# Performance work log

Hardware: AMD Instinct MI355X
Metric: run time of the kernel (lower is better)

Reference implementation:

```python
import jax, jax.numpy as jnp
import numpy as np

N, E, D, H, C = 50000, 800000, 128, 2, 128
NEG_SLOPE = 0.2
EPS = 1e-16  # matches pyg softmax denominator epsilon


def _xavier(k, shape):
    fan_out, fan_in = shape[0], shape[-1]
    lim = float(np.sqrt(6.0 / (fan_in + fan_out)))
    return jax.random.uniform(k, shape, jnp.float32, -lim, lim)


def setup_inputs() -> dict:
    key = jax.random.key(0)
    ks = jax.random.split(key, 10)
    x = jax.random.normal(ks[0], (N, D), jnp.float32)
    edge_index = jax.random.randint(ks[1], (2, E), 0, N, dtype=jnp.int64)
    W1 = _xavier(ks[2], (H * C, D))
    att_l1 = _xavier(ks[3], (H, C))
    att_r1 = _xavier(ks[4], (H, C))
    W2 = _xavier(ks[5], (H * C, H * C))
    att_l2 = _xavier(ks[6], (H, C))
    att_r2 = _xavier(ks[7], (H, C))
    Wp1 = _xavier(ks[8], (C, H * C))
    bp1 = jnp.zeros((C,), jnp.float32)
    Wp2 = _xavier(ks[9], (C, C))
    bp2 = jnp.zeros((C,), jnp.float32)
    return dict(x=x, edge_index=edge_index, W1=W1, att_l1=att_l1, att_r1=att_r1,
                W2=W2, att_l2=att_l2, att_r2=att_r2, Wp1=Wp1, bp1=bp1, Wp2=Wp2, bp2=bp2)


def gat_layer(x, W, att_l, att_r, src, dst):
    n = x.shape[0]
    xl = (x @ W.T).reshape(n, H, C)              # lin_l == lin_r (shared)
    alpha_l = (xl * att_l).sum(-1)               # [n, H]
    alpha_r = (xl * att_r).sum(-1)               # [n, H]
    # per-edge attention logits: alpha_j (source) + alpha_i (dest)
    e = jax.nn.leaky_relu(alpha_l[src] + alpha_r[dst], NEG_SLOPE)  # [E, H]
    # segment softmax over incoming edges of each destination node
    m = jax.ops.segment_max(e, dst, num_segments=n)
    m = jnp.where(jnp.isfinite(m), m, 0.0)
    ex = jnp.exp(e - m[dst])
    denom = jax.ops.segment_sum(ex, dst, num_segments=n)
    a = ex / (denom[dst] + EPS)                  # [E, H]
    # weighted message + scatter-sum aggregation
    out = jax.ops.segment_sum(a[:, :, None] * xl[src], dst, num_segments=n)
    return out.reshape(n, H * C)


def reference(x, edge_index, W1, att_l1, att_r1, W2, att_l2, att_r2, Wp1, bp1, Wp2, bp2):
    src, dst = edge_index[0], edge_index[1]
    h = jax.nn.relu(gat_layer(x, W1, att_l1, att_r1, src, dst))   # dropout p=0 -> no-op
    h = jax.nn.relu(gat_layer(h, W2, att_l2, att_r2, src, dst))
    h = h @ Wp1.T + bp1
    h = h @ Wp2.T + bp2
    return h
```

## Files before the change

### kernel.cpp

```cpp
#include <hip/hip_runtime.h>
#include <hip/hip_bf16.h>
#include <stdint.h>

#define HC 256
#define NEG_SLOPE 0.2f
#define SOFTMAX_EPS 1e-16f
#define CSR_CAP 6144
#define PART_EPB 2048

typedef float floatx4 __attribute__((ext_vector_type(4)));
typedef _Float16 half8v __attribute__((ext_vector_type(8)));

__device__ __forceinline__ float in_load(const void* p, int i, int is_bf16) {
    return is_bf16 ? (float)((const __bf16*)p)[i] : ((const float*)p)[i];
}

__device__ __forceinline__ int edge_is64(const int* ei) {
    const uint32_t* ew = (const uint32_t*)ei;
    uint32_t myw = ew[2 * (threadIdx.x & 63) + 1];
    return (__ballot(myw != 0u) == 0ull) ? 1 : 0;
}
__device__ __forceinline__ int edge_src(const int* ei, int E, int e, int is64) {
    return is64 ? ei[2 * (size_t)e] : ei[e];
}
__device__ __forceinline__ int edge_dst(const int* ei, int E, int e, int is64) {
    return is64 ? ei[2 * (size_t)E + 2 * (size_t)e] : ei[(size_t)E + e];
}

__global__ void prep_partition_kernel(
    const void* __restrict__ xin, _Float16* __restrict__ x16, int nx,
    const void* __restrict__ w1,  _Float16* __restrict__ W1f, int n1,
    const void* __restrict__ w2,  _Float16* __restrict__ W2f, int n2,
    const void* __restrict__ wp1, _Float16* __restrict__ Wp1f, int n3,
    const void* __restrict__ wp2, _Float16* __restrict__ Wp2f, int n4,
    const void* __restrict__ a0, float* __restrict__ o0, int m0,
    const void* __restrict__ a1, float* __restrict__ o1, int m1,
    const void* __restrict__ a2, float* __restrict__ o2, int m2,
    const void* __restrict__ a3, float* __restrict__ o3, int m3,
    const void* __restrict__ a4, float* __restrict__ o4, int m4,
    const void* __restrict__ a5, float* __restrict__ o5, int m5,
    const int* __restrict__ ei, int E,
    int* __restrict__ bcnt, uint2* __restrict__ stage,
    int part_blocks) {
    if (blockIdx.x < part_blocks) {
        __shared__ int hist[256];
        __shared__ int chunk[256];
        const int t = threadIdx.x;
        const int is64 = edge_is64(ei);
        const int ebase = blockIdx.x * PART_EPB;
        hist[t] = 0;
        __syncthreads();
        for (int i = t; i < PART_EPB; i += 256) {
            const int e = ebase + i;
            if (e < E) atomicAdd(&hist[edge_dst(ei, E, e, is64) >> 8], 1);
        }
        __syncthreads();
        const int h = hist[t];
        if (h > 0) chunk[t] = atomicAdd(&bcnt[t * 16], h);
        __syncthreads();
        hist[t] = 0;
        __syncthreads();
        for (int i = t; i < PART_EPB; i += 256) {
            const int e = ebase + i;
            if (e < E) {
                const int s = edge_src(ei, E, e, is64);
                const int d = edge_dst(ei, E, e, is64);
                const int b = d >> 8;
                const int local = atomicAdd(&hist[b], 1);
                const int pos = chunk[b] + local;
                if (pos < CSR_CAP)
                    stage[(size_t)b * CSR_CAP + pos] =
                        make_uint2((uint32_t)s, (uint32_t)(d & 255));
            }
        }
        return;
    }
    const uint32_t w = ((const uint32_t*)xin)[threadIdx.x & 63];
    const uint32_t ef = ((w & 0xFFFFu) >> 7) & 0xFFu;
    const int fb = (__popcll(__ballot(ef >= 90u && ef <= 135u)) > 48) ? 1 : 0;

    int off = (blockIdx.x - part_blocks) * blockDim.x + threadIdx.x;
    if (off < nx) { x16[off] = (_Float16)in_load(xin, off, fb); return; }
    off -= nx;
    if (off < n1) { W1f[off] = (_Float16)in_load(w1, off, fb); return; }
    off -= n1;
    if (off < n2) { W2f[off] = (_Float16)in_load(w2, off, fb); return; }
    off -= n2;
    if (off < n3) { Wp1f[off] = (_Float16)in_load(wp1, off, fb); return; }
    off -= n3;
    if (off < n4) { Wp2f[off] = (_Float16)in_load(wp2, off, fb); return; }
    off -= n4;
    if (off < m0) { o0[off] = in_load(a0, off, fb); return; }
    off -= m0;
    if (off < m1) { o1[off] = in_load(a1, off, fb); return; }
    off -= m1;
    if (off < m2) { o2[off] = in_load(a2, off, fb); return; }
    off -= m2;
    if (off < m3) { o3[off] = in_load(a3, off, fb); return; }
    off -= m3;
    if (off < m4) { o4[off] = in_load(a4, off, fb); return; }
    off -= m4;
    if (off < m5) { o5[off] = in_load(a5, off, fb); return; }
}

__global__ __launch_bounds__(1024) void bucket_csr_kernel(
    const int* __restrict__ bcnt, const uint2* __restrict__ stage,
    int* __restrict__ row_ptr, int* __restrict__ esrc, int nb, int N) {
    __shared__ int scanv[256];
    __shared__ int hist[256];
    __shared__ int fill[256];
    __shared__ int wsum[4], wpre[4];
    const int b = blockIdx.x;
    const int t = threadIdx.x;
    const int lane = t & 63;
    const int wv = t >> 6;

    if (t < 256) {
        const int v = (t < nb) ? min(bcnt[t * 16], CSR_CAP) : 0;
        int inc = v;
#pragma unroll
        for (int off = 1; off < 64; off <<= 1) {
            int y = __shfl_up(inc, off);
            if (lane >= off) inc += y;
        }
        if (lane == 63) wsum[wv] = inc;
        __syncthreads();
        if (t == 0) {
            int run = 0;
#pragma unroll
            for (int ww = 0; ww < 4; ww++) { wpre[ww] = run; run += wsum[ww]; }
        }
        __syncthreads();
        const int excl = wpre[wv] + inc - v;
        scanv[t] = excl;
        if (b == 0 && t == nb - 1) row_ptr[N] = excl + v;
        hist[t] = 0;
    } else {
        __syncthreads();
        __syncthreads();
    }
    __syncthreads();

    const int base = scanv[b];
    const int cnt = min(bcnt[b * 16], CSR_CAP);
    const uint2* st = stage + (size_t)b * CSR_CAP;

    for (int i = t; i < cnt; i += 1024) atomicAdd(&hist[st[i].y], 1);
    __syncthreads();
    if (t < 256) {
        const int hv = hist[t];
        int hinc = hv;
#pragma unroll
        for (int off = 1; off < 64; off <<= 1) {
            int y = __shfl_up(hinc, off);
            if (lane >= off) hinc += y;
        }
        if (lane == 63) wsum[wv] = hinc;
        __syncthreads();
        if (t == 0) {
            int run = 0;
#pragma unroll
            for (int ww = 0; ww < 4; ww++) { wpre[ww] = run; run += wsum[ww]; }
        }
        __syncthreads();
        const int hexcl = wpre[wv] + hinc - hv;
        fill[t] = hexcl;
        const int node = (b << 8) + t;
        if (node < N) row_ptr[node] = base + hexcl;
    } else {
        __syncthreads();
        __syncthreads();
    }
    __syncthreads();
    for (int i = t; i < cnt; i += 1024) {
        const uint2 e = st[i];
        const int pos = atomicAdd(&fill[e.y], 1);
        esrc[base + pos] = (int)e.x;
    }
}

template <int KTEMP, int OTILES, bool BIAS, bool ALPHA, int OMODE>
__global__ __launch_bounds__(256, 2) void gemm_bt(
    const _Float16* __restrict__ A, const _Float16* __restrict__ B,
    const float* __restrict__ bias,
    float* __restrict__ C, _Float16* __restrict__ Cf16,
    const float* __restrict__ attl, const float* __restrict__ attr,
    float* __restrict__ al, float* __restrict__ ar,
    int M) {
    static_assert(!ALPHA || OTILES == 16, "alpha fusion assumes O=256");
    constexpr int TW = OTILES / 4;
    constexpr int O = OTILES * 16;
    const int tid = threadIdx.x;
    const int lane = tid & 63;
    const int wave = tid >> 6;
    const int mbase = blockIdx.x * 64;
    const int l15 = lane & 15;
    const int q = lane >> 4;
    const int kq = q * 8;
    const int wc = wave * TW * 16;

    int arow[4];
#pragma unroll
    for (int rt = 0; rt < 4; rt++) arow[rt] = min(mbase + rt * 16 + l15, M - 1);

    floatx4 acc[4][TW];
#pragma unroll
    for (int rt = 0; rt < 4; rt++)
#pragma unroll
        for (int tt = 0; tt < TW; tt++) acc[rt][tt] = (floatx4){0.f, 0.f, 0.f, 0.f};

    constexpr int KSTEPS = KTEMP / 32;
#pragma unroll
    for (int ks = 0; ks < KSTEPS; ks++) {
        const int k0 = ks * 32;
        half8v af[4], bf[TW];
#pragma unroll
        for (int rt = 0; rt < 4; rt++)
            af[rt] = *(const half8v*)(A + (size_t)arow[rt] * KTEMP + k0 + kq);
#pragma unroll
        for (int tt = 0; tt < TW; tt++)
            bf[tt] = *(const half8v*)(B + (size_t)(wc + tt * 16 + l15) * KTEMP + k0 + kq);
#pragma unroll
        for (int rt = 0; rt < 4; rt++)
#pragma unroll
            for (int tt = 0; tt < TW; tt++)
                acc[rt][tt] = __builtin_amdgcn_mfma_f32_16x16x32_f16(af[rt], bf[tt], acc[rt][tt], 0, 0, 0);
    }

    float aLp[4][4], aRp[4][4];
    if constexpr (ALPHA) {
#pragma unroll
        for (int rt = 0; rt < 4; rt++)
#pragma unroll
            for (int r = 0; r < 4; r++) { aLp[rt][r] = 0.f; aRp[rt][r] = 0.f; }
    }

#pragma unroll
    for (int rt = 0; rt < 4; rt++) {
        const int rb = mbase + rt * 16 + q * 4;
#pragma unroll
        for (int tt = 0; tt < TW; tt++) {
            const int gcol = wc + tt * 16 + l15;
            float atlv = 0.f, atrv = 0.f;
            if constexpr (ALPHA) { atlv = attl[gcol]; atrv = attr[gcol]; }
#pragma unroll
            for (int r = 0; r < 4; r++) {
                float v = acc[rt][tt][r];
                if constexpr (BIAS) v += bias[gcol];
                if constexpr (ALPHA) { aLp[rt][r] += v * atlv; aRp[rt][r] += v * atrv; }
                const int grow = rb + r;
                if (grow < M) {
                    if constexpr (OMODE == 2) {
                        Cf16[(size_t)grow * O + gcol] = (_Float16)v;
                    } else {
                        C[(size_t)grow * O + gcol] = v;
                    }
                }
            }
        }
    }

    if constexpr (ALPHA) {
        __shared__ float sAL[4][64], sAR[4][64];
#pragma unroll
        for (int rt = 0; rt < 4; rt++)
#pragma unroll
            for (int r = 0; r < 4; r++) {
                float vl = aLp[rt][r], vr = aRp[rt][r];
                vl += __shfl_xor(vl, 1); vl += __shfl_xor(vl, 2);
                vl += __shfl_xor(vl, 4); vl += __shfl_xor(vl, 8);
                vr += __shfl_xor(vr, 1); vr += __shfl_xor(vr, 2);
                vr += __shfl_xor(vr, 4); vr += __shfl_xor(vr, 8);
                if (l15 == 0) {
                    sAL[wave][rt * 16 + q * 4 + r] = vl;
                    sAR[wave][rt * 16 + q * 4 + r] = vr;
                }
            }
        __syncthreads();
        if (tid < 64) {
            const int grow = mbase + tid;
            if (grow < M) {
                al[2 * grow]     = sAL[0][tid] + sAL[1][tid];
                al[2 * grow + 1] = sAL[2][tid] + sAL[3][tid];
                ar[2 * grow]     = sAR[0][tid] + sAR[1][tid];
                ar[2 * grow + 1] = sAR[2][tid] + sAR[3][tid];
            }
        }
    }
}

__global__ __launch_bounds__(256, 2) void proj_fused_kernel(
    const _Float16* __restrict__ A, const _Float16* __restrict__ B1,
    const float* __restrict__ b1, const _Float16* __restrict__ B2,
    const float* __restrict__ b2, float* __restrict__ out, int M) {
    __shared__ _Float16 plds[64 * 128];
    const int tid = threadIdx.x;
    const int lane = tid & 63;
    const int wave = tid >> 6;
    const int mbase = blockIdx.x * 64;
    const int l15 = lane & 15;
    const int q = lane >> 4;
    const int kq = q * 8;
    const int wc = wave * 32;

    int arow[4];
#pragma unroll
    for (int rt = 0; rt < 4; rt++) arow[rt] = min(mbase + rt * 16 + l15, M - 1);

    floatx4 acc[4][2];
#pragma unroll
    for (int rt = 0; rt < 4; rt++)
#pragma unroll
        for (int tt = 0; tt < 2; tt++) acc[rt][tt] = (floatx4){0.f, 0.f, 0.f, 0.f};
#pragma unroll
    for (int ks = 0; ks < 8; ks++) {
        const int k0 = ks * 32;
        half8v af[4], bf[2];
#pragma unroll
        for (int rt = 0; rt < 4; rt++)
            af[rt] = *(const half8v*)(A + (size_t)arow[rt] * 256 + k0 + kq);
#pragma unroll
        for (int tt = 0; tt < 2; tt++)
            bf[tt] = *(const half8v*)(B1 + (size_t)(wc + tt * 16 + l15) * 256 + k0 + kq);
#pragma unroll
        for (int rt = 0; rt < 4; rt++)
#pragma unroll
            for (int tt = 0; tt < 2; tt++)
                acc[rt][tt] = __builtin_amdgcn_mfma_f32_16x16x32_f16(af[rt], bf[tt], acc[rt][tt], 0, 0, 0);
    }
#pragma unroll
    for (int rt = 0; rt < 4; rt++) {
#pragma unroll
        for (int tt = 0; tt < 2; tt++) {
            const int col = wc + tt * 16 + l15;
            const float bv = b1[col];
#pragma unroll
            for (int r = 0; r < 4; r++) {
                const int row = rt * 16 + q * 4 + r;
                const int byt = row * 256 + ((((col >> 3) ^ (row & 15)) << 4)) + (col & 7) * 2;
                *(_Float16*)((char*)plds + byt) = (_Float16)(acc[rt][tt][r] + bv);
            }
        }
    }
    __syncthreads();

    floatx4 acc2[4][2];
#pragma unroll
    for (int rt = 0; rt < 4; rt++)
#pragma unroll
        for (int tt = 0; tt < 2; tt++) acc2[rt][tt] = (floatx4){0.f, 0.f, 0.f, 0.f};
#pragma unroll
    for (int ks = 0; ks < 4; ks++) {
        half8v af[4], bf[2];
#pragma unroll
        for (int rt = 0; rt < 4; rt++) {
            const int row = rt * 16 + l15;
            const int byt = (row << 8) + (((ks * 4 + q) ^ l15) << 4);
            af[rt] = *(const half8v*)((const char*)plds + byt);
        }
#pragma unroll
        for (int tt = 0; tt < 2; tt++)
            bf[tt] = *(const half8v*)(B2 + (size_t)(wc + tt * 16 + l15) * 128 + ks * 32 + kq);
#pragma unroll
        for (int rt = 0; rt < 4; rt++)
#pragma unroll
            for (int tt = 0; tt < 2; tt++)
                acc2[rt][tt] = __builtin_amdgcn_mfma_f32_16x16x32_f16(af[rt], bf[tt], acc2[rt][tt], 0, 0, 0);
    }
#pragma unroll
    for (int rt = 0; rt < 4; rt++) {
        const int rb = mbase + rt * 16 + q * 4;
#pragma unroll
        for (int tt = 0; tt < 2; tt++) {
            const int gcol = wc + tt * 16 + l15;
            const float bv = b2[gcol];
#pragma unroll
            for (int r = 0; r < 4; r++) {
                const int grow = rb + r;
                if (grow < M) out[(size_t)grow * 128 + gcol] = acc2[rt][tt][r] + bv;
            }
        }
    }
}

__global__ __launch_bounds__(256) void agg_fused_kernel(
    const _Float16* __restrict__ xl,
    const float* __restrict__ al, const float* __restrict__ ar,
    const int* __restrict__ row_ptr, const int* __restrict__ esrc,
    _Float16* __restrict__ hout, int N) {
    const int wid = (blockIdx.x * 256 + threadIdx.x) >> 6;
    if (wid >= N) return;
    const int lane = threadIdx.x & 63;
    const int half = lane >> 5;
    const int c8 = (lane & 31) * 8;
    const int hsel = c8 >> 7;
    const int hshift = hsel << 4;
    const int s0 = row_ptr[wid], e0 = row_ptr[wid + 1];
    const float ar0 = ar[2 * wid], ar1 = ar[2 * wid + 1];

    float acc[8];
#pragma unroll
    for (int c = 0; c < 8; c++) acc[c] = 0.f;
    float l0 = 0.f, l1 = 0.f;

    for (int base = s0; base < e0; base += 64) {
        const int n = min(64, e0 - base);
        int s = 0;
        float p0 = 0.f, p1 = 0.f;
        if (lane < n) {
            s = esrc[base + lane];
            float2 av = *(const float2*)(al + 2 * s);
            float lg0 = av.x + ar0; lg0 = lg0 > 0.f ? lg0 : NEG_SLOPE * lg0;
            float lg1 = av.y + ar1; lg1 = lg1 > 0.f ? lg1 : NEG_SLOPE * lg1;
            p0 = __expf(__builtin_fminf(lg0, 10.f));
            p1 = __expf(__builtin_fminf(lg1, 10.f));
        }
        auto pk2 = __builtin_amdgcn_cvt_pkrtz(p0, p1);
        const uint32_t pku = __builtin_bit_cast(uint32_t, pk2);
        l0 += (float)pk2[0];
        l1 += (float)pk2[1];

#pragma unroll 8
        for (int j = 0; j < n; j += 2) {
            const int jj = j + half;
            const uint32_t w32 = (uint32_t)__shfl((int)pku, jj);
            const int ss = __shfl(s, jj);
            const unsigned short wb = (unsigned short)(w32 >> hshift);
            const float wf = (float)__builtin_bit_cast(_Float16, wb);
            half8v xv = *(const half8v*)(xl + (size_t)ss * HC + c8);
#pragma unroll
            for (int c = 0; c < 8; c++) acc[c] += wf * (float)xv[c];
        }
    }

#pragma unroll
    for (int off = 1; off < 64; off <<= 1) {
        l0 += __shfl_xor(l0, off);
        l1 += __shfl_xor(l1, off);
    }
    const float winv = 1.f / ((hsel ? l1 : l0) + SOFTMAX_EPS);

#pragma unroll
    for (int c = 0; c < 8; c++) {
        acc[c] += __shfl_xor(acc[c], 32);
        acc[c] = fmaxf(acc[c] * winv, 0.f);
    }
    if (half == 0) {
        half8v vo;
#pragma unroll
        for (int c = 0; c < 8; c++) vo[c] = (_Float16)acc[c];
        *(half8v*)(hout + (size_t)wid * HC + c8) = vo;
    }
}

extern "C" void kernel_launch(void* const* d_in, const int* in_sizes, int n_in,
                              void* d_out, int out_size, void* d_ws, size_t ws_size,
                              hipStream_t stream) {
    const int D = 128;
    const int N = in_sizes[0] / D;
    const int E = in_sizes[1] / 2;
    const int* ei = (const int*)d_in[1];
    const int NBUCK = (N + 255) >> 8;

    char* w = (char*)d_ws;
    auto alloc = [&](size_t bytes) {
        void* p = w;
        w += (bytes + 255) & ~(size_t)255;
        return p;
    };
    _Float16* x16    = (_Float16*)alloc((size_t)N * D * 2);
    _Float16* W1f    = (_Float16*)alloc((size_t)in_sizes[2] * 2);
    _Float16* W2f    = (_Float16*)alloc((size_t)in_sizes[5] * 2);
    _Float16* Wp1f   = (_Float16*)alloc((size_t)in_sizes[8] * 2);
    _Float16* Wp2f   = (_Float16*)alloc((size_t)in_sizes[10] * 2);
    float*    atl1   = (float*)   alloc((size_t)in_sizes[3] * 4);
    float*    atr1   = (float*)   alloc((size_t)in_sizes[4] * 4);
    float*    atl2   = (float*)   alloc((size_t)in_sizes[6] * 4);
    float*    atr2   = (float*)   alloc((size_t)in_sizes[7] * 4);
    float*    bfp1   = (float*)   alloc((size_t)in_sizes[9] * 4);
    float*    bfp2   = (float*)   alloc((size_t)in_sizes[11] * 4);
    _Float16* xl16   = (_Float16*)alloc((size_t)N * HC * 2);
    _Float16* h16    = (_Float16*)alloc((size_t)N * HC * 2);
    float*    al     = (float*)   alloc((size_t)N * 2 * 4);
    float*    ar     = (float*)   alloc((size_t)N * 2 * 4);
    int*      row_ptr= (int*)     alloc((size_t)(N + 1) * 4);
    int*      esrc   = (int*)     alloc((size_t)E * 4);
    int*      bcnt   = (int*)     alloc((size_t)NBUCK * 16 * 4);
    uint2*    stage  = (uint2*)   alloc((size_t)NBUCK * CSR_CAP * 8);

    const int GM = (N + 63) / 64;
    const int AGG_B = (N + 3) / 4;
    const int PART_B = (E + PART_EPB - 1) / PART_EPB;

    (void)hipMemsetAsync(bcnt, 0, (size_t)NBUCK * 16 * 4, stream);
    {
        int ntot = in_sizes[0] + in_sizes[2] + in_sizes[5] + in_sizes[8] + in_sizes[10]
                 + in_sizes[3] + in_sizes[4] + in_sizes[6] + in_sizes[7]
                 + in_sizes[9] + in_sizes[11];
        int prep_blocks = (ntot + 255) / 256;
        prep_partition_kernel<<<PART_B + prep_blocks, 256, 0, stream>>>(
            d_in[0], x16, in_sizes[0],
            d_in[2], W1f, in_sizes[2],
            d_in[5], W2f, in_sizes[5],
            d_in[8], Wp1f, in_sizes[8],
            d_in[10], Wp2f, in_sizes[10],
            d_in[3], atl1, in_sizes[3],
            d_in[4], atr1, in_sizes[4],
            d_in[6], atl2, in_sizes[6],
            d_in[7], atr2, in_sizes[7],
            d_in[9], bfp1, in_sizes[9],
            d_in[11], bfp2, in_sizes[11],
            ei, E, bcnt, stage, PART_B);
    }

    bucket_csr_kernel<<<NBUCK, 1024, 0, stream>>>(bcnt, stage, row_ptr, esrc, NBUCK, N);

    gemm_bt<128, 16, false, true, 2><<<GM, 256, 0, stream>>>(
        x16, W1f, nullptr, nullptr, xl16, atl1, atr1, al, ar, N);
    agg_fused_kernel<<<AGG_B, 256, 0, stream>>>(xl16, al, ar, row_ptr, esrc, h16, N);

    gemm_bt<256, 16, false, true, 2><<<GM, 256, 0, stream>>>(
        h16, W2f, nullptr, nullptr, xl16, atl2, atr2, al, ar, N);
    agg_fused_kernel<<<AGG_B, 256, 0, stream>>>(xl16, al, ar, row_ptr, esrc, h16, N);

    proj_fused_kernel<<<GM, 256, 0, stream>>>(
        h16, Wp1f, bfp1, Wp2f, bfp2, (float*)d_out, N);
}
```

Measured before the change: 339.8 us.

## Cache edge pairs in LDS during partition and split aggregation into two launches

The partition kernel now loads each edge's source and destination once into shared memory during the histogram pass and reuses them in the scatter pass, so the edge list is not read from global memory twice. Separately, each aggregation kernel is split into two launches that cover the lower and upper halves of the nodes. The LDS cache adds 16 KB of shared memory per block, which may lower occupancy of the prep kernel. The split adds an extra launch per layer with no clear benefit, since both halves run serially on the same stream.

```diff
diff --git a/kernel.cpp b/kernel.cpp
--- a/kernel.cpp
+++ b/kernel.cpp
@@ -45,6 +45,7 @@
     if (blockIdx.x < part_blocks) {
         __shared__ int hist[256];
         __shared__ int chunk[256];
+        __shared__ uint2 eLDS[PART_EPB];
         const int t = threadIdx.x;
         const int is64 = edge_is64(ei);
         const int ebase = blockIdx.x * PART_EPB;
@@ -52,7 +53,13 @@
         __syncthreads();
         for (int i = t; i < PART_EPB; i += 256) {
             const int e = ebase + i;
-            if (e < E) atomicAdd(&hist[edge_dst(ei, E, e, is64) >> 8], 1);
+            uint2 sd = make_uint2(0u, 0xFFFFFFFFu);
+            if (e < E) {
+                sd.x = (uint32_t)edge_src(ei, E, e, is64);
+                sd.y = (uint32_t)edge_dst(ei, E, e, is64);
+                atomicAdd(&hist[sd.y >> 8], 1);
+            }
+            eLDS[i] = sd;
         }
         __syncthreads();
         const int h = hist[t];
@@ -61,16 +68,14 @@
         hist[t] = 0;
         __syncthreads();
         for (int i = t; i < PART_EPB; i += 256) {
-            const int e = ebase + i;
-            if (e < E) {
-                const int s = edge_src(ei, E, e, is64);
-                const int d = edge_dst(ei, E, e, is64);
-                const int b = d >> 8;
+            const uint2 sd = eLDS[i];
+            if (sd.y != 0xFFFFFFFFu) {
+                const int b = (int)(sd.y >> 8);
                 const int local = atomicAdd(&hist[b], 1);
                 const int pos = chunk[b] + local;
                 if (pos < CSR_CAP)
                     stage[(size_t)b * CSR_CAP + pos] =
-                        make_uint2((uint32_t)s, (uint32_t)(d & 255));
+                        make_uint2(sd.x, sd.y & 255u);
             }
         }
         return;
@@ -387,9 +392,9 @@
     const _Float16* __restrict__ xl,
     const float* __restrict__ al, const float* __restrict__ ar,
     const int* __restrict__ row_ptr, const int* __restrict__ esrc,
-    _Float16* __restrict__ hout, int N) {
-    const int wid = (blockIdx.x * 256 + threadIdx.x) >> 6;
-    if (wid >= N) return;
+    _Float16* __restrict__ hout, int nlo, int nhi) {
+    const int wid = nlo + ((blockIdx.x * 256 + threadIdx.x) >> 6);
+    if (wid >= nhi) return;
     const int lane = threadIdx.x & 63;
     const int half = lane >> 5;
     const int c8 = (lane & 31) * 8;
@@ -489,7 +494,9 @@
     uint2*    stage  = (uint2*)   alloc((size_t)NBUCK * CSR_CAP * 8);
 
     const int GM = (N + 63) / 64;
-    const int AGG_B = (N + 3) / 4;
+    const int NH = N / 2;
+    const int AGG_B1 = (NH + 3) / 4;
+    const int AGG_B2 = (N - NH + 3) / 4;
     const int PART_B = (E + PART_EPB - 1) / PART_EPB;
 
     (void)hipMemsetAsync(bcnt, 0, (size_t)NBUCK * 16 * 4, stream);
@@ -517,11 +524,13 @@
 
     gemm_bt<128, 16, false, true, 2><<<GM, 256, 0, stream>>>(
         x16, W1f, nullptr, nullptr, xl16, atl1, atr1, al, ar, N);
-    agg_fused_kernel<<<AGG_B, 256, 0, stream>>>(xl16, al, ar, row_ptr, esrc, h16, N);
+    agg_fused_kernel<<<AGG_B1, 256, 0, stream>>>(xl16, al, ar, row_ptr, esrc, h16, 0, NH);
+    agg_fused_kernel<<<AGG_B2, 256, 0, stream>>>(xl16, al, ar, row_ptr, esrc, h16, NH, N);
 
     gemm_bt<256, 16, false, true, 2><<<GM, 256, 0, stream>>>(
         h16, W2f, nullptr, nullptr, xl16, atl2, atr2, al, ar, N);
-    agg_fused_kernel<<<AGG_B, 256, 0, stream>>>(xl16, al, ar, row_ptr, esrc, h16, N);
+    agg_fused_kernel<<<AGG_B1, 256, 0, stream>>>(xl16, al, ar, row_ptr, esrc, h16, 0, NH);
+    agg_fused_kernel<<<AGG_B2, 256, 0, stream>>>(xl16, al, ar, row_ptr, esrc, h16, NH, N);
 
     proj_fused_kernel<<<GM, 256, 0, stream>>>(
         h16, Wp1f, bfp1, Wp2f, bfp2, (float*)d_out, N);
```

Result: slower. 353.8 us (+4.1%).
